# Kernel tuning notes

Measured on AMD Instinct MI355X. Metric: run time of the kernel, lower is better.

## Reference

```python
import math
import jax, jax.numpy as jnp
import numpy as np


def setup_inputs() -> dict:
    B, MA, ME = 512, 64, 256
    d_model, d_qk, N = 256, 32, 200000
    rng = np.random.default_rng(0)
    actor_len = rng.integers(1, MA + 1, B)
    actee_len = rng.integers(1, ME + 1, B)
    # flat scatter positions: indices(1) + indices(0) * max_len
    qindices = np.concatenate([np.arange(l) + i * MA for i, l in enumerate(actor_len)]).astype(np.int64)
    kindices = np.concatenate([np.arange(l) + i * ME for i, l in enumerate(actee_len)]).astype(np.int64)
    A, E = len(qindices), len(kindices)
    actors = rng.integers(0, N, A)            # absolute indices into x (offsets pre-applied)
    actees = rng.integers(0, N, E)
    # previous action for each actor must index a valid actee of its env
    prev_actions = rng.integers(0, np.repeat(actee_len, actor_len))
    key = jax.random.key(0)
    k0, k1, k2 = jax.random.split(key, 3)
    s = 1.0 / math.sqrt(d_model)
    return {
        "x": jax.random.normal(k0, (N, d_model), jnp.float32),
        "Wq": jax.random.normal(k1, (d_model, d_qk), jnp.float32) * s,
        "bq": jnp.zeros((d_qk,), jnp.float32),
        "Wk": jax.random.normal(k2, (d_model, d_qk), jnp.float32) * s,
        "bk": jnp.zeros((d_qk,), jnp.float32),
        "actors": jnp.asarray(actors, jnp.int32),
        "qindices": jnp.asarray(qindices, jnp.int32),
        "actees": jnp.asarray(actees, jnp.int32),
        "kindices": jnp.asarray(kindices, jnp.int32),
        "prev_actions": jnp.asarray(prev_actions, jnp.int32),
        "B": B, "max_actors": MA, "max_actees": ME,
    }


def reference(x, Wq, bq, Wk, bk, actors, qindices, actees, kindices, prev_actions, B, max_actors, max_actees):
    d_qk = Wq.shape[1]
    scale = 1.0 / math.sqrt(d_qk)
    queries = x[actors] @ Wq + bq                         # [A, d_qk] ragged gather + project
    keys = x[actees] @ Wk + bk                            # [E, d_qk]
    # scatter into zero-padded (queries) / one-padded (keys) buffers
    pq = jnp.zeros((B * max_actors, d_qk), x.dtype).at[qindices].set(queries).reshape(B, max_actors, d_qk)
    qmask = jnp.zeros((B * max_actors,), x.dtype).at[qindices].set(1.0).reshape(B, max_actors)
    pk = jnp.ones((B * max_actees, d_qk), x.dtype).at[kindices].set(keys).reshape(B, max_actees, d_qk)
    kmask = jnp.zeros((B * max_actees,), x.dtype).at[kindices].set(1.0).reshape(B, max_actees)
    logits = jnp.einsum("bqd,bkd->bqk", pq, pk) * scale   # [B, max_actors, max_actees]
    valid = qmask[:, :, None] * kmask[:, None, :]
    logits = jnp.where(valid == 0, jnp.asarray(-1e9, x.dtype), logits)
    # prev_actions branch: scatter actions into one-padded buffer
    padded_actions = jnp.ones((B * max_actors,), jnp.int32).at[qindices].set(prev_actions).reshape(B, max_actors)
    logp = jax.nn.log_softmax(logits, axis=-1)
    logprob = jnp.take_along_axis(logp, padded_actions[:, :, None], axis=-1)[..., 0]  # [B, max_actors]
    entropy = -jnp.sum(jnp.exp(logp) * logp, axis=-1)
    # gather-back to ragged layout
    return (
        padded_actions.reshape(-1)[qindices],
        logprob.reshape(-1)[qindices],
        entropy.reshape(-1)[qindices],
        logits,
    )
```

## Files before the change

kernel.cpp:

```cpp
#include <hip/hip_runtime.h>
#include <math.h>

#define MA 64
#define ME 256
#define DM 256
#define DQK 32
#define ENVSTRIDE (MA * ME)
#define MASKVAL -998244352.0f
#define QK_SCALE 0.17677669529663687f
#define KSTR 40

typedef __attribute__((ext_vector_type(8))) short bf16x8;
typedef __attribute__((ext_vector_type(4))) float f32x4;
typedef unsigned short u16;

__device__ __forceinline__ int lb(const int* __restrict__ a, int n, int v){
  int lo = 0, hi = n;
  while (lo < hi){ int mid = (lo + hi) >> 1; if (a[mid] < v) lo = mid + 1; else hi = mid; }
  return lo;
}
__device__ __forceinline__ unsigned pk2bf(float lo, float hi){
  unsigned ul = __float_as_uint(lo); ul = ul + 0x7FFFu + ((ul >> 16) & 1u);
  unsigned uh = __float_as_uint(hi); uh = uh + 0x7FFFu + ((uh >> 16) & 1u);
  return (ul >> 16) | (uh & 0xFFFF0000u);
}
__device__ __forceinline__ u16 f2bu(float f){
  unsigned u = __float_as_uint(f);
  return (u16)((u + 0x7FFFu + ((u >> 16) & 1u)) >> 16);
}

__device__ __forceinline__ void load_wfrag(const float* __restrict__ W, int lr, int lq,
                                           bf16x8 (*bfr)[2]){
  #pragma unroll
  for (int kk = 0; kk < 8; ++kk) {
    const int k0 = kk * 32 + lq * 8;
    #pragma unroll
    for (int nt = 0; nt < 2; ++nt) {
      const float* wp = W + (size_t)k0 * DQK + nt * 16 + lr;
      union { unsigned u[4]; bf16x8 v; } fb;
      #pragma unroll
      for (int p = 0; p < 4; ++p) fb.u[p] = pk2bf(wp[(2*p)*DQK], wp[(2*p+1)*DQK]);
      bfr[kk][nt] = fb.v;
    }
  }
}

__device__ __forceinline__ void proj_tile(const float* __restrict__ x,
                                          const int* __restrict__ gath, int start, int len,
                                          int rbase, int lr, int lq,
                                          const bf16x8 (*bfr)[2], float bv0, float bv1,
                                          u16* __restrict__ dst){
  const int arow = start + min(rbase + lr, len - 1);
  const float* xr = x + (size_t)gath[arow] * DM + lq * 8;
  f32x4 a0 = {bv0, bv0, bv0, bv0}, a1 = {bv1, bv1, bv1, bv1};
  #pragma unroll
  for (int kk = 0; kk < 8; ++kk) {
    float4 c0 = *(const float4*)(xr + kk * 32);
    float4 c1 = *(const float4*)(xr + kk * 32 + 4);
    union { unsigned u[4]; bf16x8 v; } fa;
    fa.u[0] = pk2bf(c0.x, c0.y); fa.u[1] = pk2bf(c0.z, c0.w);
    fa.u[2] = pk2bf(c1.x, c1.y); fa.u[3] = pk2bf(c1.z, c1.w);
    a0 = __builtin_amdgcn_mfma_f32_16x16x32_bf16(fa.v, bfr[kk][0], a0, 0, 0, 0);
    a1 = __builtin_amdgcn_mfma_f32_16x16x32_bf16(fa.v, bfr[kk][1], a1, 0, 0, 0);
  }
  #pragma unroll
  for (int reg = 0; reg < 4; ++reg) {
    const int row = rbase + 4 * lq + reg;
    if (row < len) {
      dst[row * KSTR + lr]      = f2bu(a0[reg]);
      dst[row * KSTR + 16 + lr] = f2bu(a1[reg]);
    }
  }
}

__global__ __launch_bounds__(256)
void fused_env(const float* __restrict__ x,  const float* __restrict__ Wq, const float* __restrict__ bq,
               const float* __restrict__ Wk, const float* __restrict__ bk,
               const int* __restrict__ actors, const int* __restrict__ qindices,
               const int* __restrict__ actees, const int* __restrict__ kindices,
               const int* __restrict__ prev_actions, int A, int E, float* __restrict__ out)
{
  __shared__ u16 kb[ME * KSTR];
  __shared__ u16 qsm[MA * KSTR];
  __shared__ int srange[4];

  const int t = threadIdx.x, b = blockIdx.x;
  if (t < 4) {
    const int* arr = (t < 2) ? qindices : kindices;
    const int nn = (t < 2) ? A : E;
    const int vv = (t == 0) ? b * MA : (t == 1) ? (b + 1) * MA
                 : (t == 2) ? b * ME : (b + 1) * ME;
    srange[t] = lb(arr, nn, vv);
  }
  __syncthreads();
  const int qstart = srange[0], qlen = srange[1] - srange[0];
  const int kstart = srange[2], klen = srange[3] - srange[2];

  const int lane = t & 63, w = t >> 6;
  const int lr = lane & 15, lq = lane >> 4;

  if (16 * w < klen) {
    bf16x8 bfr[8][2];
    load_wfrag(Wk, lr, lq, bfr);
    const float bv0 = bk[lr], bv1 = bk[16 + lr];
    #pragma unroll
    for (int i = 0; i < 4; ++i) {
      const int rbase = 16 * w + 64 * i;
      if (rbase < klen)
        proj_tile(x, actees, kstart, klen, rbase, lr, lq, bfr, bv0, bv1, kb);
    }
  }
  if (16 * w < qlen) {
    bf16x8 bfr[8][2];
    load_wfrag(Wq, lr, lq, bfr);
    proj_tile(x, actors, qstart, qlen, 16 * w, lr, lq, bfr, bq[lr], bq[16 + lr], qsm);
  }
  __syncthreads();

  float* out_lg = out + (size_t)3 * A + (size_t)b * ENVSTRIDE;
  const int row0 = 16 * w;

  if (row0 >= qlen) {
    const float4 mv = make_float4(MASKVAL, MASKVAL, MASKVAL, MASKVAL);
    float4* o4 = (float4*)out_lg;
    #pragma unroll
    for (int rr = 0; rr < 16; ++rr) o4[(row0 + rr) * 64 + lane] = mv;
    return;
  }

  const bf16x8 afr = *(const bf16x8*)&qsm[(row0 + lr) * KSTR + lq * 8];
  f32x4 acc[16];
  #pragma unroll
  for (int nt = 0; nt < 16; ++nt) {
    const bf16x8 bfr2 = *(const bf16x8*)&kb[(16 * nt + lr) * KSTR + lq * 8];
    f32x4 z = {0.f, 0.f, 0.f, 0.f};
    acc[nt] = __builtin_amdgcn_mfma_f32_16x16x32_bf16(afr, bfr2, z, 0, 0, 0);
  }

  int par[4];
  float m[4], spa[4], es[4], ts[4];
  #pragma unroll
  for (int reg = 0; reg < 4; ++reg) {
    const int r = row0 + 4 * lq + reg;
    par[reg] = (r < qlen) ? (prev_actions[qstart + r] & (ME - 1)) : -1;
    m[reg] = MASKVAL; spa[reg] = MASKVAL; es[reg] = 0.f; ts[reg] = 0.f;
  }

  #pragma unroll
  for (int nt = 0; nt < 16; ++nt) {
    const int col = 16 * nt + lr;
    const bool kv = (col < klen);
    #pragma unroll
    for (int reg = 0; reg < 4; ++reg) {
      const float d = kv ? acc[nt][reg] * QK_SCALE : MASKVAL;
      acc[nt][reg] = d;
      m[reg] = fmaxf(m[reg], d);
      if (col == par[reg]) spa[reg] = d;
    }
  }
  #pragma unroll
  for (int off = 1; off < 16; off <<= 1) {
    #pragma unroll
    for (int reg = 0; reg < 4; ++reg) {
      m[reg]   = fmaxf(m[reg],   __shfl_xor(m[reg],   off));
      spa[reg] = fmaxf(spa[reg], __shfl_xor(spa[reg], off));
    }
  }
  #pragma unroll
  for (int nt = 0; nt < 16; ++nt) {
    #pragma unroll
    for (int reg = 0; reg < 4; ++reg) {
      const float dd = acc[nt][reg] - m[reg];
      if (dd > -80.f) { const float e = __expf(dd); es[reg] += e; ts[reg] += e * dd; }
    }
  }
  #pragma unroll
  for (int off = 1; off < 16; off <<= 1) {
    #pragma unroll
    for (int reg = 0; reg < 4; ++reg) {
      es[reg] += __shfl_xor(es[reg], off);
      ts[reg] += __shfl_xor(ts[reg], off);
    }
  }

  #pragma unroll
  for (int nt = 0; nt < 16; ++nt) {
    #pragma unroll
    for (int reg = 0; reg < 4; ++reg) {
      const int r = row0 + 4 * lq + reg;
      out_lg[r * ME + 16 * nt + lr] = (r < qlen) ? acc[nt][reg] : MASKVAL;
    }
  }
  if (lr == 0) {
    #pragma unroll
    for (int reg = 0; reg < 4; ++reg) {
      const int r = row0 + 4 * lq + reg;
      if (r < qlen) {
        const float lS = __logf(fmaxf(es[reg], 1e-30f));
        out[qstart + r]         = (float)par[reg];
        out[A + qstart + r]     = spa[reg] - m[reg] - lS;
        out[2 * A + qstart + r] = lS - ts[reg] / es[reg];
      }
    }
  }
}

extern "C" void kernel_launch(void* const* d_in, const int* in_sizes, int n_in,
                              void* d_out, int out_size, void* d_ws, size_t ws_size,
                              hipStream_t stream) {
  const float* x  = (const float*)d_in[0];
  const float* Wq = (const float*)d_in[1];
  const float* bq = (const float*)d_in[2];
  const float* Wk = (const float*)d_in[3];
  const float* bk = (const float*)d_in[4];
  const int* actors       = (const int*)d_in[5];
  const int* qindices     = (const int*)d_in[6];
  const int* actees       = (const int*)d_in[7];
  const int* kindices     = (const int*)d_in[8];
  const int* prev_actions = (const int*)d_in[9];

  const int A = in_sizes[5];
  const int E = in_sizes[7];
  const int B = (out_size - 3 * A) / ENVSTRIDE;
  if (B <= 0) return;

  fused_env<<<dim3(B), dim3(256), 0, stream>>>(
      x, Wq, bq, Wk, bk, actors, qindices, actees, kindices, prev_actions,
      A, E, (float*)d_out);
}
```

Measured before the change: 41.28 us.

## Stage bf16 weight fragments in LDS and balance projection tiles across waves

All 256 threads now cooperatively convert Wq and Wk to bf16 MFMA fragments once per block and store them in shared memory, replacing per-wave register fragment loads. Key and query projection tiles are placed in one combined list that the four waves take in round-robin order, so work no longer piles onto the waves that also handle query rows. Each tile issues all of its x loads up front before the MFMAs to increase memory-level parallelism. This adds 32KB of LDS per block, which may reduce occupancy, and every block now pays for the full weight conversion.

```diff
diff --git a/kernel.cpp b/kernel.cpp
--- a/kernel.cpp
+++ b/kernel.cpp
@@ -29,50 +29,6 @@
   return (u16)((u + 0x7FFFu + ((u >> 16) & 1u)) >> 16);
 }
 
-__device__ __forceinline__ void load_wfrag(const float* __restrict__ W, int lr, int lq,
-                                           bf16x8 (*bfr)[2]){
-  #pragma unroll
-  for (int kk = 0; kk < 8; ++kk) {
-    const int k0 = kk * 32 + lq * 8;
-    #pragma unroll
-    for (int nt = 0; nt < 2; ++nt) {
-      const float* wp = W + (size_t)k0 * DQK + nt * 16 + lr;
-      union { unsigned u[4]; bf16x8 v; } fb;
-      #pragma unroll
-      for (int p = 0; p < 4; ++p) fb.u[p] = pk2bf(wp[(2*p)*DQK], wp[(2*p+1)*DQK]);
-      bfr[kk][nt] = fb.v;
-    }
-  }
-}
-
-__device__ __forceinline__ void proj_tile(const float* __restrict__ x,
-                                          const int* __restrict__ gath, int start, int len,
-                                          int rbase, int lr, int lq,
-                                          const bf16x8 (*bfr)[2], float bv0, float bv1,
-                                          u16* __restrict__ dst){
-  const int arow = start + min(rbase + lr, len - 1);
-  const float* xr = x + (size_t)gath[arow] * DM + lq * 8;
-  f32x4 a0 = {bv0, bv0, bv0, bv0}, a1 = {bv1, bv1, bv1, bv1};
-  #pragma unroll
-  for (int kk = 0; kk < 8; ++kk) {
-    float4 c0 = *(const float4*)(xr + kk * 32);
-    float4 c1 = *(const float4*)(xr + kk * 32 + 4);
-    union { unsigned u[4]; bf16x8 v; } fa;
-    fa.u[0] = pk2bf(c0.x, c0.y); fa.u[1] = pk2bf(c0.z, c0.w);
-    fa.u[2] = pk2bf(c1.x, c1.y); fa.u[3] = pk2bf(c1.z, c1.w);
-    a0 = __builtin_amdgcn_mfma_f32_16x16x32_bf16(fa.v, bfr[kk][0], a0, 0, 0, 0);
-    a1 = __builtin_amdgcn_mfma_f32_16x16x32_bf16(fa.v, bfr[kk][1], a1, 0, 0, 0);
-  }
-  #pragma unroll
-  for (int reg = 0; reg < 4; ++reg) {
-    const int row = rbase + 4 * lq + reg;
-    if (row < len) {
-      dst[row * KSTR + lr]      = f2bu(a0[reg]);
-      dst[row * KSTR + 16 + lr] = f2bu(a1[reg]);
-    }
-  }
-}
-
 __global__ __launch_bounds__(256)
 void fused_env(const float* __restrict__ x,  const float* __restrict__ Wq, const float* __restrict__ bq,
                const float* __restrict__ Wk, const float* __restrict__ bk,
@@ -80,6 +36,7 @@
                const int* __restrict__ actees, const int* __restrict__ kindices,
                const int* __restrict__ prev_actions, int A, int E, float* __restrict__ out)
 {
+  __shared__ __align__(16) unsigned wfr32[2 * 8 * 2 * 256];
   __shared__ u16 kb[ME * KSTR];
   __shared__ u16 qsm[MA * KSTR];
   __shared__ int srange[4];
@@ -92,28 +49,72 @@
                  : (t == 2) ? b * ME : (b + 1) * ME;
     srange[t] = lb(arr, nn, vv);
   }
+
+  #pragma unroll
+  for (int ii = 0; ii < 32; ++ii) {
+    const int i = t + ii * 256;
+    const int p = i & 3, ln = (i >> 2) & 63, nt = (i >> 8) & 1, kk = (i >> 9) & 7, wh = i >> 12;
+    const int k0  = kk * 32 + (ln >> 4) * 8 + 2 * p;
+    const int col = nt * 16 + (ln & 15);
+    const float* W = wh ? Wq : Wk;
+    wfr32[i] = pk2bf(W[(size_t)k0 * DQK + col], W[(size_t)(k0 + 1) * DQK + col]);
+  }
   __syncthreads();
+
   const int qstart = srange[0], qlen = srange[1] - srange[0];
   const int kstart = srange[2], klen = srange[3] - srange[2];
 
   const int lane = t & 63, w = t >> 6;
   const int lr = lane & 15, lq = lane >> 4;
 
-  if (16 * w < klen) {
-    bf16x8 bfr[8][2];
-    load_wfrag(Wk, lr, lq, bfr);
-    const float bv0 = bk[lr], bv1 = bk[16 + lr];
-    #pragma unroll
-    for (int i = 0; i < 4; ++i) {
-      const int rbase = 16 * w + 64 * i;
-      if (rbase < klen)
-        proj_tile(x, actees, kstart, klen, rbase, lr, lq, bfr, bv0, bv1, kb);
-    }
-  }
-  if (16 * w < qlen) {
-    bf16x8 bfr[8][2];
-    load_wfrag(Wq, lr, lq, bfr);
-    proj_tile(x, actors, qstart, qlen, 16 * w, lr, lq, bfr, bq[lr], bq[16 + lr], qsm);
+  const float bkv0 = bk[lr], bkv1 = bk[16 + lr];
+  const float bqv0 = bq[lr], bqv1 = bq[16 + lr];
+
+  const int kt = (klen + 15) >> 4;
+  const int qt = (qlen + 15) >> 4;
+  const int ntiles = kt + qt;
+
+  for (int i = w; i < ntiles; i += 4) {
+    const bool isk = (i < kt);
+    const int  rbase = isk ? (i << 4) : ((i - kt) << 4);
+    const int  len   = isk ? klen : qlen;
+    const int  start = isk ? kstart : qstart;
+    const int* gath  = isk ? actees : actors;
+    u16*       dst   = isk ? kb : qsm;
+    const unsigned* fbase = &wfr32[(isk ? 0 : 4096) + lane * 4];
+
+    const int arow = start + min(rbase + lr, len - 1);
+    const float* xr = x + (size_t)gath[arow] * DM + lq * 8;
+
+    float4 cx[16];
+    #pragma unroll
+    for (int kk = 0; kk < 8; ++kk) {
+      cx[2*kk]   = *(const float4*)(xr + kk * 32);
+      cx[2*kk+1] = *(const float4*)(xr + kk * 32 + 4);
+    }
+
+    const float v0 = isk ? bkv0 : bqv0, v1 = isk ? bkv1 : bqv1;
+    f32x4 a0 = {v0, v0, v0, v0}, a1 = {v1, v1, v1, v1};
+    #pragma unroll
+    for (int kk = 0; kk < 8; ++kk) {
+      union { unsigned u[4]; bf16x8 v; } fa;
+      fa.u[0] = pk2bf(cx[2*kk].x,   cx[2*kk].y);
+      fa.u[1] = pk2bf(cx[2*kk].z,   cx[2*kk].w);
+      fa.u[2] = pk2bf(cx[2*kk+1].x, cx[2*kk+1].y);
+      fa.u[3] = pk2bf(cx[2*kk+1].z, cx[2*kk+1].w);
+      const bf16x8 b0 = *(const bf16x8*)(fbase + kk * 512);
+      const bf16x8 b1 = *(const bf16x8*)(fbase + kk * 512 + 256);
+      a0 = __builtin_amdgcn_mfma_f32_16x16x32_bf16(fa.v, b0, a0, 0, 0, 0);
+      a1 = __builtin_amdgcn_mfma_f32_16x16x32_bf16(fa.v, b1, a1, 0, 0, 0);
+    }
+    #pragma unroll
+    for (int reg = 0; reg < 4; ++reg) {
+      const int row = rbase + 4 * lq + reg;
+      if (row < len) {
+        dst[row * KSTR + lr]      = f2bu(a0[reg]);
+        dst[row * KSTR + 16 + lr] = f2bu(a1[reg]);
+      }
+    }
   }
   __syncthreads();
 
```

New measurement: 41.06 us. Within noise of the previous version (-0.5%).

## Stage gathered rows into LDS asynchronously with double buffering and prepacked weights

Applied to the files above, without the earlier changes.

Adds a small pre-kernel that converts Wk/Wq to bf16 MFMA fragment layout once, so each block loads fragments directly instead of converting them. Gathered x rows are now copied into swizzled LDS buffers with global_load_lds and double-buffered per wave, overlapping the next tile's gather with the current tile's MFMA projection. Key and query tiles are distributed round-robin across all four waves to balance work. The staging buffers add about 128KB of LDS per block, which limits residency to one block per CU, and the extra launch adds overhead.

```diff
diff --git a/kernel.cpp b/kernel.cpp
--- a/kernel.cpp
+++ b/kernel.cpp
@@ -29,34 +29,45 @@
   return (u16)((u + 0x7FFFu + ((u >> 16) & 1u)) >> 16);
 }
 
-__device__ __forceinline__ void load_wfrag(const float* __restrict__ W, int lr, int lq,
-                                           bf16x8 (*bfr)[2]){
+__global__ __launch_bounds__(256)
+void pack_w(const float* __restrict__ Wk, const float* __restrict__ Wq,
+            unsigned* __restrict__ wfr_g){
+  const int base = blockIdx.x * 512 + threadIdx.x;
+  #pragma unroll
+  for (int ii = 0; ii < 2; ++ii) {
+    const int i = base + ii * 256;
+    const int p = i & 3, ln = (i >> 2) & 63, nt = (i >> 8) & 1, kk = (i >> 9) & 7, wh = i >> 12;
+    const int k0  = kk * 32 + (ln >> 4) * 8 + 2 * p;
+    const int col = nt * 16 + (ln & 15);
+    const float* W = wh ? Wq : Wk;
+    wfr_g[i] = pk2bf(W[(size_t)k0 * DQK + col], W[(size_t)(k0 + 1) * DQK + col]);
+  }
+}
+
+__device__ __forceinline__ void stage_tile(const float* __restrict__ x, int idxv,
+                                           int lane, float* sb){
+  #pragma unroll
+  for (int s = 0; s < 16; ++s) {
+    const int row = __shfl(idxv, s);
+    const char* gp = (const char*)(x + (size_t)row * DM) + ((lane * 16) ^ ((s & 7) << 4));
+    __builtin_amdgcn_global_load_lds(
+        (const __attribute__((address_space(1))) void*)gp,
+        (__attribute__((address_space(3))) void*)(sb + s * 256),
+        16, 0, 0);
+  }
+}
+
+__device__ __forceinline__ void compute_tile(const float* sb, int lr, int lq,
+                                             const bf16x8 (&bfr)[8][2], float bv0, float bv1,
+                                             int rbase, int len, u16* __restrict__ dst){
+  const char* sbB = (const char*)sb + (size_t)lr * 1024;
+  const int sw = (lr & 7) << 4;
+  f32x4 a0 = {bv0, bv0, bv0, bv0}, a1 = {bv1, bv1, bv1, bv1};
   #pragma unroll
   for (int kk = 0; kk < 8; ++kk) {
-    const int k0 = kk * 32 + lq * 8;
-    #pragma unroll
-    for (int nt = 0; nt < 2; ++nt) {
-      const float* wp = W + (size_t)k0 * DQK + nt * 16 + lr;
-      union { unsigned u[4]; bf16x8 v; } fb;
-      #pragma unroll
-      for (int p = 0; p < 4; ++p) fb.u[p] = pk2bf(wp[(2*p)*DQK], wp[(2*p+1)*DQK]);
-      bfr[kk][nt] = fb.v;
-    }
-  }
-}
-
-__device__ __forceinline__ void proj_tile(const float* __restrict__ x,
-                                          const int* __restrict__ gath, int start, int len,
-                                          int rbase, int lr, int lq,
-                                          const bf16x8 (*bfr)[2], float bv0, float bv1,
-                                          u16* __restrict__ dst){
-  const int arow = start + min(rbase + lr, len - 1);
-  const float* xr = x + (size_t)gath[arow] * DM + lq * 8;
-  f32x4 a0 = {bv0, bv0, bv0, bv0}, a1 = {bv1, bv1, bv1, bv1};
-  #pragma unroll
-  for (int kk = 0; kk < 8; ++kk) {
-    float4 c0 = *(const float4*)(xr + kk * 32);
-    float4 c1 = *(const float4*)(xr + kk * 32 + 4);
+    const int p0 = kk * 128 + lq * 32;
+    const float4 c0 = *(const float4*)(sbB + ((p0)      ^ sw));
+    const float4 c1 = *(const float4*)(sbB + ((p0 + 16) ^ sw));
     union { unsigned u[4]; bf16x8 v; } fa;
     fa.u[0] = pk2bf(c0.x, c0.y); fa.u[1] = pk2bf(c0.z, c0.w);
     fa.u[2] = pk2bf(c1.x, c1.y); fa.u[3] = pk2bf(c1.z, c1.w);
@@ -74,17 +85,23 @@
 }
 
 __global__ __launch_bounds__(256)
-void fused_env(const float* __restrict__ x,  const float* __restrict__ Wq, const float* __restrict__ bq,
-               const float* __restrict__ Wk, const float* __restrict__ bk,
+void fused_env(const float* __restrict__ x,
+               const float* __restrict__ bq, const float* __restrict__ bk,
                const int* __restrict__ actors, const int* __restrict__ qindices,
                const int* __restrict__ actees, const int* __restrict__ kindices,
-               const int* __restrict__ prev_actions, int A, int E, float* __restrict__ out)
+               const int* __restrict__ prev_actions,
+               const unsigned* __restrict__ wfr_g,
+               int A, int E, float* __restrict__ out)
 {
+  __shared__ float stg[4][2][4096];
   __shared__ u16 kb[ME * KSTR];
   __shared__ u16 qsm[MA * KSTR];
   __shared__ int srange[4];
 
   const int t = threadIdx.x, b = blockIdx.x;
+  const int lane = t & 63, w = t >> 6;
+  const int lr = lane & 15, lq = lane >> 4;
+
   if (t < 4) {
     const int* arr = (t < 2) ? qindices : kindices;
     const int nn = (t < 2) ? A : E;
@@ -96,24 +113,51 @@
   const int qstart = srange[0], qlen = srange[1] - srange[0];
   const int kstart = srange[2], klen = srange[3] - srange[2];
 
-  const int lane = t & 63, w = t >> 6;
-  const int lr = lane & 15, lq = lane >> 4;
-
-  if (16 * w < klen) {
-    bf16x8 bfr[8][2];
-    load_wfrag(Wk, lr, lq, bfr);
-    const float bv0 = bk[lr], bv1 = bk[16 + lr];
-    #pragma unroll
-    for (int i = 0; i < 4; ++i) {
-      const int rbase = 16 * w + 64 * i;
-      if (rbase < klen)
-        proj_tile(x, actees, kstart, klen, rbase, lr, lq, bfr, bv0, bv1, kb);
-    }
-  }
-  if (16 * w < qlen) {
-    bf16x8 bfr[8][2];
-    load_wfrag(Wq, lr, lq, bfr);
-    proj_tile(x, actors, qstart, qlen, 16 * w, lr, lq, bfr, bq[lr], bq[16 + lr], qsm);
+  bf16x8 bfrK[8][2], bfrQ[8][2];
+  {
+    const unsigned* fbK = wfr_g + lane * 4;
+    const unsigned* fbQ = wfr_g + 4096 + lane * 4;
+    #pragma unroll
+    for (int kk = 0; kk < 8; ++kk) {
+      bfrK[kk][0] = *(const bf16x8*)(fbK + kk * 512);
+      bfrK[kk][1] = *(const bf16x8*)(fbK + kk * 512 + 256);
+      bfrQ[kk][0] = *(const bf16x8*)(fbQ + kk * 512);
+      bfrQ[kk][1] = *(const bf16x8*)(fbQ + kk * 512 + 256);
+    }
+  }
+  const float bkv0 = bk[lr], bkv1 = bk[16 + lr];
+  const float bqv0 = bq[lr], bqv1 = bq[16 + lr];
+
+  const int kt = (klen + 15) >> 4;
+  const int qt = (qlen + 15) >> 4;
+  const int nt_ = kt + qt;
+  const int nw = (nt_ > w) ? ((nt_ - w + 3) >> 2) : 0;
+
+  int idxv[6];
+  #pragma unroll
+  for (int tt = 0; tt < 6; ++tt) {
+    const int ic  = min(w + 4 * tt, nt_ - 1);
+    const bool isk = ic < kt;
+    const int rbase = (isk ? ic : ic - kt) << 4;
+    const int len   = isk ? klen : qlen;
+    const int start = isk ? kstart : qstart;
+    const int* gi   = isk ? actees : actors;
+    idxv[tt] = (lane < 16) ? gi[start + min(rbase + lane, len - 1)] : 0;
+  }
+
+  #pragma unroll
+  for (int tt = 0; tt < 6; ++tt) {
+    if (tt < nw)
+      stage_tile(x, idxv[tt], lane, &stg[w][tt & 1][0]);
+    if (tt >= 1 && (tt - 1) < nw) {
+      if (tt < nw) { asm volatile("s_waitcnt vmcnt(16)" ::: "memory"); }
+      else         { asm volatile("s_waitcnt vmcnt(0)"  ::: "memory"); }
+      const int ip = w + 4 * (tt - 1);
+      const bool pk = ip < kt;
+      const int rb = (pk ? ip : ip - kt) << 4;
+      if (pk) compute_tile(&stg[w][(tt - 1) & 1][0], lr, lq, bfrK, bkv0, bkv1, rb, klen, kb);
+      else    compute_tile(&stg[w][(tt - 1) & 1][0], lr, lq, bfrQ, bqv0, bqv1, rb, qlen, qsm);
+    }
   }
   __syncthreads();
 
@@ -224,7 +268,10 @@
   const int B = (out_size - 3 * A) / ENVSTRIDE;
   if (B <= 0) return;
 
+  unsigned* wfr_g = (unsigned*)d_ws;
+
+  pack_w<<<dim3(16), dim3(256), 0, stream>>>(Wk, Wq, wfr_g);
   fused_env<<<dim3(B), dim3(256), 0, stream>>>(
-      x, Wq, bq, Wk, bk, actors, qindices, actees, kindices, prev_actions,
-      A, E, (float*)d_out);
-}
+      x, bq, bk, actors, qindices, actees, kindices, prev_actions,
+      wfr_g, A, E, (float*)d_out);
+}
```

Result: slower. 53.21 us (+28.9%).
